# Optimization experiments

Hardware: AMD Instinct MI355X
Metric: run time of the kernel (lower is better)

Reference implementation:

```python
import jax, jax.numpy as jnp
import numpy as np

# Module constants (from init_kwargs + mp_num=8 from the mesh)
D_MODEL = 1024
N_HEAD = 16
D_HEAD = 64
D_ROT = 64
MP = 8
B, S = 2, 2048
LOCAL = N_HEAD * D_HEAD // MP          # 128 : per-mp-shard qkv dim
F_IN = N_HEAD * D_HEAD * 3 + D_MODEL * 8  # 11264 : fused qkv+ff projection width
D_OUT_IN = D_MODEL + 4 * D_MODEL       # 5120 : attn (1024) + glu (4096) into output_proj
LN_EPS = 1e-5


def _rotate_every_two(x):
    # x: [..., d] with d even -> interleaved (-x2, x1)
    x1 = x[..., ::2]
    x2 = x[..., 1::2]
    return jnp.stack((-x2, x1), axis=-1).reshape(*x.shape[:-1], -1)


def _fixed_pos_embedding(seq_len, dim):
    inv_freq = 1.0 / (10000.0 ** (np.arange(0, dim, 2) / dim))
    t = np.einsum('i,j->ij', np.arange(seq_len), inv_freq)  # [S, dim//2]
    return jnp.asarray(np.sin(t), jnp.float32), jnp.asarray(np.cos(t), jnp.float32)


def _apply_rotary(x, sin, cos):
    # x: [B, S, mp, D_ROT]; sin/cos: [S, D_ROT//2]
    sin = jnp.repeat(sin, 2, axis=-1)[-x.shape[-3]:, None, :]  # [S,1,D_ROT]
    cos = jnp.repeat(cos, 2, axis=-1)[-x.shape[-3]:, None, :]
    return x * cos + _rotate_every_two(x) * sin


def setup_inputs() -> dict:
    key = jax.random.key(0)
    ks = jax.random.split(key, 4)
    x = jax.random.normal(ks[0], (B, S, D_MODEL), jnp.float32)
    attn_bias = jnp.zeros((1, S, S), jnp.float32)
    ln_scale = jnp.ones((D_MODEL,), jnp.float32)
    ln_offset = jnp.zeros((D_MODEL,), jnp.float32)
    w_in = jax.random.normal(ks[1], (D_MODEL, F_IN), jnp.float32) / np.sqrt(D_MODEL)
    b_in = jnp.zeros((F_IN,), jnp.float32)
    w_out = jax.random.normal(ks[2], (D_OUT_IN, D_MODEL), jnp.float32) / np.sqrt(D_MODEL)
    b_out = jnp.zeros((D_MODEL,), jnp.float32)
    return {"x": x, "attn_bias": attn_bias, "ln_scale": ln_scale, "ln_offset": ln_offset,
            "w_in": w_in, "b_in": b_in, "w_out": w_out, "b_out": b_out}


def reference(x, attn_bias, ln_scale, ln_offset, w_in, b_in, w_out, b_out):
    b, s, d = x.shape
    # LayerNorm (create_scale=True, create_offset=True, eps=1e-5)
    mu = jnp.mean(x, axis=-1, keepdims=True)
    var = jnp.var(x, axis=-1, keepdims=True)
    h = (x - mu) * jax.lax.rsqrt(var + LN_EPS) * ln_scale + ln_offset
    # fused QKV + FF projection, then mp split: [B,S,mp,F_IN/mp]
    proj = (h @ w_in + b_in).reshape(b, s, MP, -1)
    q, v, k, ff = jnp.split(proj, [LOCAL, 2 * LOCAL, 3 * LOCAL], axis=-1)
    # rotary on the first D_ROT dims of each mp shard (head_split is a shape no-op)
    sin, cos = _fixed_pos_embedding(s, D_ROT)
    q = jnp.concatenate([_apply_rotary(q[..., :D_ROT], sin, cos), q[..., D_ROT:]], axis=-1)
    k = jnp.concatenate([_apply_rotary(k[..., :D_ROT], sin, cos), k[..., D_ROT:]], axis=-1)
    # attention over h=mp shard-heads of dim LOCAL; scaled by sqrt(d_head) per source
    scale = np.sqrt(D_HEAD).astype(x.dtype)
    logits = jnp.einsum('bthd,bThd->bhtT', q, k) / scale  # [B,MP,S,S]
    causal = jnp.tril(jnp.ones((s, s), x.dtype))[None]
    bias = -1e10 * (1.0 - causal) + attn_bias
    weights = jax.nn.softmax(logits + bias, axis=-1)
    attn_vec = jnp.einsum('bhtT,bThd->bthd', weights, v)  # [B,S,MP,LOCAL]
    # GLU FFN (jax.nn.gelu default = tanh approximation, as in source)
    ff_out, ff_gate = jnp.split(ff, 2, axis=-1)
    glu = ff_out * jax.nn.gelu(ff_gate)  # [B,S,MP,4*D_MODEL/MP]
    # output: concat per-shard then flatten -> output_proj
    out = jnp.concatenate([attn_vec, glu], axis=-1).reshape(b, s, -1)  # [B,S,5120]
    return out @ w_out + b_out
```

## Files before the change

kernel.cpp:

```cpp
#include <hip/hip_runtime.h>
#include <stdint.h>

#define B_   2
#define S_   2048
#define DM   1024
#define FIN  11264
#define DOUT 5120
#define NSH  8
#define DH   128
#define ROWS (B_*S_)

typedef __attribute__((ext_vector_type(8))) __bf16 bf16x8;
typedef __attribute__((ext_vector_type(4))) __bf16 bf16x4;
typedef __attribute__((ext_vector_type(4))) float  f32x4;

union U2 { unsigned int u; __bf16 h[2]; };

__device__ __forceinline__ void gload16(const void* g, void* l) {
    __builtin_amdgcn_global_load_lds((const __attribute__((address_space(1))) void*)g,
                                     (__attribute__((address_space(3))) void*)l, 16, 0, 0);
}

__global__ __launch_bounds__(256) void ln_kernel(const float* __restrict__ x,
                                                 const float* __restrict__ sc,
                                                 const float* __restrict__ of,
                                                 __bf16* __restrict__ h) {
    int row = blockIdx.x, t = threadIdx.x;
    const float4 v = *(const float4*)&x[(size_t)row*DM + t*4];
    float s  = v.x + v.y + v.z + v.w;
    float ss = v.x*v.x + v.y*v.y + v.z*v.z + v.w*v.w;
#pragma unroll
    for (int off = 32; off >= 1; off >>= 1) {
        s  += __shfl_xor(s, off);
        ss += __shfl_xor(ss, off);
    }
    __shared__ float rs_[4], rss_[4];
    int wid = t >> 6, lane = t & 63;
    if (lane == 0) { rs_[wid] = s; rss_[wid] = ss; }
    __syncthreads();
    s  = rs_[0] + rs_[1] + rs_[2] + rs_[3];
    ss = rss_[0] + rss_[1] + rss_[2] + rss_[3];
    float mu  = s * (1.f/DM);
    float var = ss * (1.f/DM) - mu*mu;
    float r   = rsqrtf(var + 1e-5f);
    float4 scv = *(const float4*)&sc[t*4];
    float4 ofv = *(const float4*)&of[t*4];
    bf16x4 o;
    o[0] = (__bf16)((v.x-mu)*r*scv.x + ofv.x);
    o[1] = (__bf16)((v.y-mu)*r*scv.y + ofv.y);
    o[2] = (__bf16)((v.z-mu)*r*scv.z + ofv.z);
    o[3] = (__bf16)((v.w-mu)*r*scv.w + ofv.w);
    *(bf16x4*)&h[(size_t)row*DM + t*4] = o;
}

__global__ __launch_bounds__(256) void transpose_kernel(const float* __restrict__ in,
                                                        __bf16* __restrict__ out,
                                                        int R, int C) {
    __shared__ __bf16 tile[64][72];
    int c0 = blockIdx.x * 64, r0 = blockIdx.y * 64;
    int t = threadIdx.x;
#pragma unroll
    for (int it = 0; it < 4; ++it) {
        int flat = it*1024 + t*4;
        int rl = flat >> 6, cl = flat & 63;
        float4 v = *(const float4*)&in[(size_t)(r0+rl)*C + c0 + cl];
        tile[rl][cl+0] = (__bf16)v.x;
        tile[rl][cl+1] = (__bf16)v.y;
        tile[rl][cl+2] = (__bf16)v.z;
        tile[rl][cl+3] = (__bf16)v.w;
    }
    __syncthreads();
#pragma unroll
    for (int it = 0; it < 4; ++it) {
        int flat = it*1024 + t*4;
        int cl = flat >> 6, rl = flat & 63;
        bf16x4 o;
#pragma unroll
        for (int j = 0; j < 4; ++j) o[j] = tile[rl+j][cl];
        *(bf16x4*)&out[(size_t)(c0+cl)*R + r0 + rl] = o;
    }
}

__global__ __launch_bounds__(256) void vtrans_kernel(const __bf16* __restrict__ in,
                                                     __bf16* __restrict__ out) {
    __shared__ __bf16 tile[64*72];
    int d0 = blockIdx.x*64, s0 = blockIdx.y*64;
    size_t base = (size_t)blockIdx.z * (size_t)S_ * DH;
    int t = threadIdx.x;
#pragma unroll
    for (int it = 0; it < 2; ++it) {
        int idx = it*2048 + t*8;
        int sl = idx >> 6, dl = idx & 63;
        bf16x8 v = *(const bf16x8*)&in[base + (size_t)(s0+sl)*DH + d0+dl];
        int ch = ((dl>>3) ^ (sl&7) ^ ((sl>>3)&7)) & 7;
        *(bf16x8*)&tile[sl*72 + ch*8] = v;
    }
    __syncthreads();
#pragma unroll
    for (int it = 0; it < 2; ++it) {
        int idx = it*2048 + t*8;
        int dl = idx >> 6, sl = idx & 63;
        bf16x8 o;
#pragma unroll
        for (int j = 0; j < 8; ++j) {
            int r = sl + j;
            int ch = ((dl>>3) ^ (r&7) ^ ((r>>3)&7)) & 7;
            o[j] = tile[r*72 + ch*8 + (dl&7)];
        }
        *(bf16x8*)&out[base + (size_t)(d0+dl)*S_ + s0 + sl] = o;
    }
}

__global__ __launch_bounds__(512, 2) void gemm256_kernel(const __bf16* __restrict__ A,
                                                         const __bf16* __restrict__ BT,
                                                         const float* __restrict__ bias,
                                                         __bf16* __restrict__ Cb,
                                                         float* __restrict__ Cf,
                                                         int M, int N, int K, int klen) {
    __shared__ __align__(16) char lds[131072];
    int t = threadIdx.x, wid = t >> 6, lane = t & 63;
    int wr = wid >> 2, wc = wid & 3;
    int fr = lane & 15, fq = lane >> 4;
    int kbeg = blockIdx.z * klen;
    int nbx = gridDim.x;
    int bid = blockIdx.y * nbx + blockIdx.x;
    int cpx = (nbx * gridDim.y) >> 3;
    int swz = (bid & 7) * cpx + (bid >> 3);
    int bx = swz % nbx, by = swz / nbx;
    int m0 = by * 256, n0 = bx * 256;

    const __bf16* pA[2];
    const __bf16* pB[2];
#pragma unroll
    for (int j = 0; j < 2; ++j) {
        int F = j*8192 + t*16;
        int row = F >> 6;
        int co  = (F & 63) ^ (((F >> 7) & 3) << 4);
        pA[j] = A  + (size_t)(m0 + row) * K + kbeg + (co >> 1);
        pB[j] = BT + (size_t)(n0 + row) * K + kbeg + (co >> 1);
    }
    int offA[8], offB[4];
#pragma unroll
    for (int i = 0; i < 8; ++i) {
        int row = wr*128 + i*16 + fr;
        offA[i] = row*64 + ((fq*16) ^ (((row >> 1) & 3) << 4));
    }
#pragma unroll
    for (int n = 0; n < 4; ++n) {
        int row = wc*64 + n*16 + fr;
        offB[n] = 16384 + row*64 + ((fq*16) ^ (((row >> 1) & 3) << 4));
    }

    f32x4 acc[8][4] = {};
    gload16(pA[0],      lds +     0 + wid*1024);
    gload16(pA[1],      lds +  8192 + wid*1024);
    gload16(pB[0],      lds + 16384 + wid*1024);
    gload16(pB[1],      lds + 24576 + wid*1024);
    gload16(pA[0] + 32, lds + 32768 +     0 + wid*1024);
    gload16(pA[1] + 32, lds + 32768 +  8192 + wid*1024);
    gload16(pB[0] + 32, lds + 32768 + 16384 + wid*1024);
    gload16(pB[1] + 32, lds + 32768 + 24576 + wid*1024);
    asm volatile("s_waitcnt vmcnt(4)" ::: "memory");
    __builtin_amdgcn_s_barrier();

    int NT = klen >> 5;
    for (int tt = 0; tt < NT; ++tt) {
        const char* sb = lds + (tt & 3) * 32768;
        bool pf = (tt + 2 < NT);
        char* sn = lds + ((tt + 2) & 3) * 32768;
        int ko = (tt + 2) << 5;
        bf16x8 a[4], b[4];
#pragma unroll
        for (int n = 0; n < 4; ++n) b[n] = *(const bf16x8*)(sb + offB[n]);
#pragma unroll
        for (int i = 0; i < 4; ++i) a[i] = *(const bf16x8*)(sb + offA[i]);
        if (pf) {
            gload16(pA[0] + ko, sn +        wid*1024);
            gload16(pA[1] + ko, sn + 8192 + wid*1024);
        }
        __builtin_amdgcn_s_barrier();
        asm volatile("s_waitcnt lgkmcnt(0)");
        __builtin_amdgcn_s_setprio(1);
#pragma unroll
        for (int i = 0; i < 4; ++i)
#pragma unroll
            for (int n = 0; n < 4; ++n)
                acc[i][n] = __builtin_amdgcn_mfma_f32_16x16x32_bf16(a[i], b[n], acc[i][n], 0, 0, 0);
        __builtin_amdgcn_s_setprio(0);
        __builtin_amdgcn_s_barrier();
#pragma unroll
        for (int i = 0; i < 4; ++i) a[i] = *(const bf16x8*)(sb + offA[4 + i]);
        if (pf) {
            gload16(pB[0] + ko, sn + 16384 + wid*1024);
            gload16(pB[1] + ko, sn + 24576 + wid*1024);
        }
        __builtin_amdgcn_s_barrier();
        asm volatile("s_waitcnt lgkmcnt(0)");
        __builtin_amdgcn_s_setprio(1);
#pragma unroll
        for (int i = 0; i < 4; ++i)
#pragma unroll
            for (int n = 0; n < 4; ++n)
                acc[4+i][n] = __builtin_amdgcn_mfma_f32_16x16x32_bf16(a[i], b[n], acc[4+i][n], 0, 0, 0);
        __builtin_amdgcn_s_setprio(0);
        if (pf)               asm volatile("s_waitcnt vmcnt(4)" ::: "memory");
        else if (tt + 1 < NT) asm volatile("s_waitcnt vmcnt(0)" ::: "memory");
        if (tt + 1 < NT) __builtin_amdgcn_s_barrier();
    }
    if (Cb) {
#pragma unroll
        for (int i = 0; i < 8; ++i)
#pragma unroll
            for (int n = 0; n < 4; ++n) {
                int col = n0 + wc*64 + n*16 + fr;
                float bv = bias[col];
#pragma unroll
                for (int r = 0; r < 4; ++r) {
                    int row = m0 + wr*128 + i*16 + fq*4 + r;
                    Cb[(size_t)row*N + col] = (__bf16)(acc[i][n][r] + bv);
                }
            }
    } else {
        float* Cz = Cf + (size_t)blockIdx.z * M * N;
#pragma unroll
        for (int i = 0; i < 8; ++i)
#pragma unroll
            for (int n = 0; n < 4; ++n) {
                int col = n0 + wc*64 + n*16 + fr;
#pragma unroll
                for (int r = 0; r < 4; ++r) {
                    int row = m0 + wr*128 + i*16 + fq*4 + r;
                    Cz[(size_t)row*N + col] = acc[i][n][r];
                }
            }
    }
}

__global__ __launch_bounds__(256) void addbias_kernel(const float* __restrict__ pk,
                                                      const float* __restrict__ bias,
                                                      float* __restrict__ out) {
    int idx = blockIdx.x * 256 + threadIdx.x;
    const size_t stride = (size_t)ROWS * DM / 4;
    float4 a0 = ((const float4*)pk)[idx];
    float4 a1 = ((const float4*)pk)[idx + stride];
    float4 a2 = ((const float4*)pk)[idx + 2*stride];
    float4 a3 = ((const float4*)pk)[idx + 3*stride];
    float4 bb = ((const float4*)bias)[idx & 255];
    float4 o;
    o.x = a0.x + a1.x + a2.x + a3.x + bb.x;
    o.y = a0.y + a1.y + a2.y + a3.y + bb.y;
    o.z = a0.z + a1.z + a2.z + a3.z + bb.z;
    o.w = a0.w + a1.w + a2.w + a3.w + bb.w;
    ((float4*)out)[idx] = o;
}

__global__ __launch_bounds__(256) void qkv_rope_kernel(const __bf16* __restrict__ proj,
                                                       __bf16* __restrict__ qh,
                                                       __bf16* __restrict__ kh,
                                                       __bf16* __restrict__ vh) {
    int idx = blockIdx.x * 256 + threadIdx.x;
    int i   = idx & 63;
    int p   = (idx >> 6) & 7;
    int row = idx >> 9;
    int s   = row & (S_ - 1);
    int b   = row >> 11;
    const __bf16* base = proj + (size_t)row*FIN + p*1408;
    int d0 = i*2;
    U2 uq, uv, uk;
    uq.u = *(const unsigned int*)&base[d0];
    uv.u = *(const unsigned int*)&base[128+d0];
    uk.u = *(const unsigned int*)&base[256+d0];
    float q0 = uq.h[0], q1 = uq.h[1];
    float v0 = uv.h[0], v1 = uv.h[1];
    float k0 = uk.h[0], k1 = uk.h[1];
    if (d0 < 64) {
        float inv = exp2f(-(float)i * 0.4152410118609203f);
        float ang = (float)s * inv;
        float cn = __cosf(ang), sn = __sinf(ang);
        float a;
        a = q0*cn - q1*sn; q1 = q1*cn + q0*sn; q0 = a;
        a = k0*cn - k1*sn; k1 = k1*cn + k0*sn; k0 = a;
    }
    size_t o = ((size_t)((b*NSH + p)*S_ + s))*DH + d0;
    U2 oq, ok, ov;
    oq.h[0] = (__bf16)(q0*0.125f); oq.h[1] = (__bf16)(q1*0.125f);
    ok.h[0] = (__bf16)k0;          ok.h[1] = (__bf16)k1;
    ov.h[0] = (__bf16)v0;          ov.h[1] = (__bf16)v1;
    *(unsigned int*)&qh[o] = oq.u;
    *(unsigned int*)&kh[o] = ok.u;
    *(unsigned int*)&vh[o] = ov.u;
}

__global__ __launch_bounds__(256) void glu_kernel(const __bf16* __restrict__ proj,
                                                  __bf16* __restrict__ ag) {
    int idx = blockIdx.x * 256 + threadIdx.x;
    int j2  = (idx & 255) * 2;
    int p   = (idx >> 8) & 7;
    int row = idx >> 11;
    const __bf16* bp = proj + (size_t)row*FIN + p*1408;
    U2 xo, xg, o;
    xo.u = *(const unsigned int*)&bp[384 + j2];
    xg.u = *(const unsigned int*)&bp[896 + j2];
#pragma unroll
    for (int j = 0; j < 2; ++j) {
        float g = xg.h[j];
        float e2 = __expf(1.5957691216057308f*(g + 0.044715f*g*g*g));
        float gl = g * (1.f - 1.f/(e2 + 1.f));
        o.h[j] = (__bf16)((float)xo.h[j] * gl);
    }
    *(unsigned int*)&ag[(size_t)row*DOUT + p*640 + 128 + j2] = o.u;
}

__device__ __forceinline__ void stage_kv(const __bf16* Kb, const __bf16* Vg,
                                         char* KsB, char* VsB,
                                         int kvbase, int t, int wid) {
#pragma unroll
    for (int j = 0; j < 4; ++j) {
        int F = (j*256 + t)*16;
        int r = F >> 8, c = F & 255;
        gload16(Kb + (size_t)(kvbase + r)*DH + ((c ^ ((r & 7) << 4)) >> 1),
                KsB + j*4096 + (wid << 10));
    }
#pragma unroll
    for (int j = 0; j < 4; ++j) {
        int F = (j*256 + t)*16;
        int r = F >> 7, c = F & 127;
        gload16(Vg + (size_t)r*S_ + kvbase + ((c ^ ((r & 7) << 4)) >> 1),
                VsB + j*4096 + (wid << 10));
    }
}

__global__ __launch_bounds__(256, 2) void attn_kernel(const __bf16* __restrict__ qh,
                                                      const __bf16* __restrict__ kh,
                                                      const __bf16* __restrict__ vt,
                                                      const float* __restrict__ ab,
                                                      __bf16* __restrict__ ag) {
    __shared__ __bf16 Ks[2*8192];
    __shared__ __bf16 Vs[2*8192];
    __shared__ __bf16 Ps[4][16*72];
    int bh = blockIdx.y;
    int b = bh >> 3, hh = bh & 7;
    int xr = blockIdx.x;
    int qb = (xr & 1) ? (31 - (xr >> 1)) : (xr >> 1);
    int q0 = qb * 64;
    int t = threadIdx.x, wid = t >> 6, lane = t & 63;
    int fr = lane & 15, fkb = (lane >> 4) * 16;
    const __bf16* Qb = qh + (size_t)bh * S_ * DH;
    const __bf16* Kb = kh + (size_t)bh * S_ * DH;
    const __bf16* Vg = vt + (size_t)bh * DH * S_;
    bf16x8 qf[4];
#pragma unroll
    for (int kk = 0; kk < 4; ++kk)
        qf[kk] = *(const bf16x8*)&Qb[(size_t)(q0 + wid*16 + fr)*DH + kk*32 + (lane>>4)*8];
    float m[4] = {-3e38f, -3e38f, -3e38f, -3e38f};
    float l[4] = {0.f, 0.f, 0.f, 0.f};
    f32x4 o[8] = {};
    int rowb = q0 + wid*16 + (lane >> 4)*4;
    int nit = qb + 1;
    stage_kv(Kb, Vg, (char*)Ks, (char*)Vs, 0, t, wid);
    for (int it = 0; it < nit; ++it) {
        int kv0 = it * 64, cur = it & 1;
        float abv[4][4];
#pragma unroll
        for (int n = 0; n < 4; ++n)
#pragma unroll
            for (int r = 0; r < 4; ++r)
                abv[n][r] = ab[(size_t)(rowb + r)*S_ + kv0 + n*16 + fr];
        if (it + 1 < nit) {
            stage_kv(Kb, Vg, (char*)Ks + (cur^1)*16384, (char*)Vs + (cur^1)*16384,
                     kv0 + 64, t, wid);
            asm volatile("s_waitcnt vmcnt(8)" ::: "memory");
        } else {
            asm volatile("s_waitcnt vmcnt(0)" ::: "memory");
        }
        __builtin_amdgcn_s_barrier();
        const char* KsC = (const char*)Ks + cur*16384;
        float pv[4][4];
        __builtin_amdgcn_s_setprio(1);
#pragma unroll
        for (int n = 0; n < 4; ++n) {
            f32x4 sacc = {};
#pragma unroll
            for (int kk = 0; kk < 4; ++kk) {
                int row = n*16 + fr;
                int c2 = (kk*64 + fkb) ^ ((fr & 7) << 4);
                bf16x8 kf = *(const bf16x8*)(KsC + row*256 + c2);
                sacc = __builtin_amdgcn_mfma_f32_16x16x32_bf16(qf[kk], kf, sacc, 0, 0, 0);
            }
#pragma unroll
            for (int r = 0; r < 4; ++r) pv[n][r] = sacc[r];
        }
        __builtin_amdgcn_s_setprio(0);
#pragma unroll
        for (int n = 0; n < 4; ++n) {
            int col = kv0 + n*16 + fr;
#pragma unroll
            for (int r = 0; r < 4; ++r)
                pv[n][r] += abv[n][r] + (col <= rowb + r ? 0.f : -1e10f);
        }
        float alpha[4];
#pragma unroll
        for (int r = 0; r < 4; ++r) {
            float mx = fmaxf(fmaxf(pv[0][r], pv[1][r]), fmaxf(pv[2][r], pv[3][r]));
#pragma unroll
            for (int off = 8; off >= 1; off >>= 1) mx = fmaxf(mx, __shfl_xor(mx, off));
            float mn = fmaxf(m[r], mx);
            alpha[r] = __expf(m[r] - mn);
            m[r] = mn;
            float sum = 0.f;
#pragma unroll
            for (int n = 0; n < 4; ++n) { pv[n][r] = __expf(pv[n][r] - mn); sum += pv[n][r]; }
#pragma unroll
            for (int off = 8; off >= 1; off >>= 1) sum += __shfl_xor(sum, off);
            l[r] = l[r]*alpha[r] + sum;
        }
#pragma unroll
        for (int nf = 0; nf < 8; ++nf)
#pragma unroll
            for (int r = 0; r < 4; ++r) o[nf][r] *= alpha[r];
#pragma unroll
        for (int n = 0; n < 4; ++n)
#pragma unroll
            for (int r = 0; r < 4; ++r)
                Ps[wid][((lane >> 4)*4 + r)*72 + n*16 + fr] = (__bf16)pv[n][r];
        asm volatile("s_waitcnt lgkmcnt(0)" ::: "memory");
        __builtin_amdgcn_sched_barrier(0);
        bf16x8 pf[2];
#pragma unroll
        for (int kk = 0; kk < 2; ++kk)
            pf[kk] = *(const bf16x8*)&Ps[wid][fr*72 + kk*32 + (lane>>4)*8];
        const char* VsC = (const char*)Vs + cur*16384;
        __builtin_amdgcn_s_setprio(1);
#pragma unroll
        for (int nf = 0; nf < 8; ++nf) {
#pragma unroll
            for (int kk = 0; kk < 2; ++kk) {
                int row = nf*16 + fr;
                int c2 = (kk*64 + fkb) ^ ((fr & 7) << 4);
                bf16x8 vf = *(const bf16x8*)(VsC + row*128 + c2);
                o[nf] = __builtin_amdgcn_mfma_f32_16x16x32_bf16(pf[kk], vf, o[nf], 0, 0, 0);
            }
        }
        __builtin_amdgcn_s_setprio(0);
        asm volatile("s_waitcnt lgkmcnt(0)" ::: "memory");
        __builtin_amdgcn_sched_barrier(0);
        __builtin_amdgcn_s_barrier();
    }
    int rq = (lane >> 4) * 4;
#pragma unroll
    for (int r = 0; r < 4; ++r) {
        float inv = 1.f / l[r];
#pragma unroll
        for (int nf = 0; nf < 8; ++nf) {
            int qr = q0 + wid*16 + rq + r;
            int d = nf*16 + fr;
            ag[((size_t)(b*S_ + qr))*DOUT + hh*640 + d] = (__bf16)(o[nf][r] * inv);
        }
    }
}

extern "C" void kernel_launch(void* const* d_in, const int* in_sizes, int n_in,
                              void* d_out, int out_size, void* d_ws, size_t ws_size,
                              hipStream_t stream) {
    const float* x     = (const float*)d_in[0];
    const float* ab    = (const float*)d_in[1];
    const float* lns   = (const float*)d_in[2];
    const float* lno   = (const float*)d_in[3];
    const float* w_in  = (const float*)d_in[4];
    const float* b_in  = (const float*)d_in[5];
    const float* w_out = (const float*)d_in[6];
    const float* b_out = (const float*)d_in[7];
    float* out = (float*)d_out;
    char* ws = (char*)d_ws;

    __bf16* w_in_t  = (__bf16*)(ws);
    __bf16* w_out_t = (__bf16*)(ws +  23068672);
    __bf16* hbuf    = (__bf16*)(ws +  33554432);
    __bf16* proj    = (__bf16*)(ws +  41943040);
    __bf16* vtb     = (__bf16*)(ws +  41943040);
    float*  pk      = (float*)(ws +  52428800);
    __bf16* qh      = (__bf16*)(ws + 134217728);
    __bf16* kh      = (__bf16*)(ws + 142606336);
    __bf16* vh      = (__bf16*)(ws + 150994944);
    __bf16* agb     = (__bf16*)(ws + 159383552);

    transpose_kernel<<<dim3(FIN/64, DM/64), 256, 0, stream>>>(w_in, w_in_t, DM, FIN);
    transpose_kernel<<<dim3(DM/64, DOUT/64), 256, 0, stream>>>(w_out, w_out_t, DOUT, DM);
    ln_kernel<<<ROWS, 256, 0, stream>>>(x, lns, lno, hbuf);
    gemm256_kernel<<<dim3(FIN/256, ROWS/256, 1), 512, 0, stream>>>(hbuf, w_in_t, b_in,
                                                                   proj, nullptr,
                                                                   ROWS, FIN, DM, DM);
    qkv_rope_kernel<<<(ROWS*8*64)/256, 256, 0, stream>>>(proj, qh, kh, vh);
    glu_kernel<<<(ROWS*8*256)/256, 256, 0, stream>>>(proj, agb);
    vtrans_kernel<<<dim3(DH/64, S_/64, B_*NSH), 256, 0, stream>>>(vh, vtb);
    attn_kernel<<<dim3(S_/64, B_*NSH), 256, 0, stream>>>(qh, kh, vtb, ab, agb);
    gemm256_kernel<<<dim3(DM/256, ROWS/256, 4), 512, 0, stream>>>(agb, w_out_t, nullptr,
                                                                  nullptr, pk,
                                                                  ROWS, DM, DOUT, DOUT/4);
    addbias_kernel<<<ROWS*DM/1024, 256, 0, stream>>>(pk, b_out, out);
}
```

Measured before the change: 319.8 us.

## Replace 256x256 pipelined GEMM with simpler 128x128 single-buffered GEMM

Result: slower. 340.4 us (+6.4%).

```diff
diff --git a/kernel.cpp b/kernel.cpp
--- a/kernel.cpp
+++ b/kernel.cpp
@@ -111,15 +111,15 @@
     }
 }
 
-__global__ __launch_bounds__(512, 2) void gemm256_kernel(const __bf16* __restrict__ A,
+__global__ __launch_bounds__(256, 4) void gemm128_kernel(const __bf16* __restrict__ A,
                                                          const __bf16* __restrict__ BT,
                                                          const float* __restrict__ bias,
                                                          __bf16* __restrict__ Cb,
                                                          float* __restrict__ Cf,
                                                          int M, int N, int K, int klen) {
-    __shared__ __align__(16) char lds[131072];
+    __shared__ __align__(16) char lds[32768];
     int t = threadIdx.x, wid = t >> 6, lane = t & 63;
-    int wr = wid >> 2, wc = wid & 3;
+    int wm = (wid >> 1) * 64, wn = (wid & 1) * 64;
     int fr = lane & 15, fq = lane >> 4;
     int kbeg = blockIdx.z * klen;
     int nbx = gridDim.x;
@@ -127,109 +127,82 @@
     int cpx = (nbx * gridDim.y) >> 3;
     int swz = (bid & 7) * cpx + (bid >> 3);
     int bx = swz % nbx, by = swz / nbx;
-    int m0 = by * 256, n0 = bx * 256;
-
-    const __bf16* pA[2];
-    const __bf16* pB[2];
-#pragma unroll
-    for (int j = 0; j < 2; ++j) {
-        int F = j*8192 + t*16;
-        int row = F >> 6;
-        int co  = (F & 63) ^ (((F >> 7) & 3) << 4);
-        pA[j] = A  + (size_t)(m0 + row) * K + kbeg + (co >> 1);
-        pB[j] = BT + (size_t)(n0 + row) * K + kbeg + (co >> 1);
-    }
-    int offA[8], offB[4];
-#pragma unroll
-    for (int i = 0; i < 8; ++i) {
-        int row = wr*128 + i*16 + fr;
-        offA[i] = row*64 + ((fq*16) ^ (((row >> 1) & 3) << 4));
-    }
-#pragma unroll
-    for (int n = 0; n < 4; ++n) {
-        int row = wc*64 + n*16 + fr;
-        offB[n] = 16384 + row*64 + ((fq*16) ^ (((row >> 1) & 3) << 4));
-    }
-
-    f32x4 acc[8][4] = {};
-    gload16(pA[0],      lds +     0 + wid*1024);
-    gload16(pA[1],      lds +  8192 + wid*1024);
-    gload16(pB[0],      lds + 16384 + wid*1024);
-    gload16(pB[1],      lds + 24576 + wid*1024);
-    gload16(pA[0] + 32, lds + 32768 +     0 + wid*1024);
-    gload16(pA[1] + 32, lds + 32768 +  8192 + wid*1024);
-    gload16(pB[0] + 32, lds + 32768 + 16384 + wid*1024);
-    gload16(pB[1] + 32, lds + 32768 + 24576 + wid*1024);
-    asm volatile("s_waitcnt vmcnt(4)" ::: "memory");
-    __builtin_amdgcn_s_barrier();
-
-    int NT = klen >> 5;
-    for (int tt = 0; tt < NT; ++tt) {
-        const char* sb = lds + (tt & 3) * 32768;
-        bool pf = (tt + 2 < NT);
-        char* sn = lds + ((tt + 2) & 3) * 32768;
-        int ko = (tt + 2) << 5;
+    int m0 = by * 128, n0 = bx * 128;
+
+    const __bf16* srcA[4];
+    const __bf16* srcB[4];
+#pragma unroll
+    for (int j = 0; j < 4; ++j) {
+        int F = (j*256 + t) * 16;
+        int row = F >> 7;
+        int c = (F & 127) ^ ((row & 7) << 4);
+        srcA[j] = A  + (size_t)(m0 + row) * K + kbeg + (c >> 1);
+        srcB[j] = BT + (size_t)(n0 + row) * K + kbeg + (c >> 1);
+    }
+    int rowA[4], rowB[4];
+#pragma unroll
+    for (int i = 0; i < 4; ++i) {
+        rowA[i] = (wm + i*16 + fr) * 128;
+        rowB[i] = 16384 + (wn + i*16 + fr) * 128;
+    }
+    int swzb = (fr & 7) << 4;
+    int cb0 = (fq*16) ^ swzb;
+    int cb1 = (64 + fq*16) ^ swzb;
+
+    f32x4 acc[4][4] = {};
+    for (int k0 = 0; k0 < klen; k0 += 64) {
+#pragma unroll
+        for (int j = 0; j < 4; ++j)
+            gload16(srcA[j] + k0, lds + j*4096 + wid*1024);
+#pragma unroll
+        for (int j = 0; j < 4; ++j)
+            gload16(srcB[j] + k0, lds + 16384 + j*4096 + wid*1024);
+        __syncthreads();
         bf16x8 a[4], b[4];
 #pragma unroll
-        for (int n = 0; n < 4; ++n) b[n] = *(const bf16x8*)(sb + offB[n]);
-#pragma unroll
-        for (int i = 0; i < 4; ++i) a[i] = *(const bf16x8*)(sb + offA[i]);
-        if (pf) {
-            gload16(pA[0] + ko, sn +        wid*1024);
-            gload16(pA[1] + ko, sn + 8192 + wid*1024);
-        }
-        __builtin_amdgcn_s_barrier();
-        asm volatile("s_waitcnt lgkmcnt(0)");
-        __builtin_amdgcn_s_setprio(1);
+        for (int i = 0; i < 4; ++i) a[i] = *(const bf16x8*)(lds + rowA[i] + cb0);
+#pragma unroll
+        for (int n = 0; n < 4; ++n) b[n] = *(const bf16x8*)(lds + rowB[n] + cb0);
 #pragma unroll
         for (int i = 0; i < 4; ++i)
 #pragma unroll
             for (int n = 0; n < 4; ++n)
                 acc[i][n] = __builtin_amdgcn_mfma_f32_16x16x32_bf16(a[i], b[n], acc[i][n], 0, 0, 0);
-        __builtin_amdgcn_s_setprio(0);
-        __builtin_amdgcn_s_barrier();
-#pragma unroll
-        for (int i = 0; i < 4; ++i) a[i] = *(const bf16x8*)(sb + offA[4 + i]);
-        if (pf) {
-            gload16(pB[0] + ko, sn + 16384 + wid*1024);
-            gload16(pB[1] + ko, sn + 24576 + wid*1024);
-        }
-        __builtin_amdgcn_s_barrier();
-        asm volatile("s_waitcnt lgkmcnt(0)");
-        __builtin_amdgcn_s_setprio(1);
+#pragma unroll
+        for (int i = 0; i < 4; ++i) a[i] = *(const bf16x8*)(lds + rowA[i] + cb1);
+#pragma unroll
+        for (int n = 0; n < 4; ++n) b[n] = *(const bf16x8*)(lds + rowB[n] + cb1);
 #pragma unroll
         for (int i = 0; i < 4; ++i)
 #pragma unroll
             for (int n = 0; n < 4; ++n)
-                acc[4+i][n] = __builtin_amdgcn_mfma_f32_16x16x32_bf16(a[i], b[n], acc[4+i][n], 0, 0, 0);
-        __builtin_amdgcn_s_setprio(0);
-        if (pf)               asm volatile("s_waitcnt vmcnt(4)" ::: "memory");
-        else if (tt + 1 < NT) asm volatile("s_waitcnt vmcnt(0)" ::: "memory");
-        if (tt + 1 < NT) __builtin_amdgcn_s_barrier();
-    }
+                acc[i][n] = __builtin_amdgcn_mfma_f32_16x16x32_bf16(a[i], b[n], acc[i][n], 0, 0, 0);
+        __syncthreads();
+    }
+    int rq = fq * 4;
     if (Cb) {
 #pragma unroll
-        for (int i = 0; i < 8; ++i)
+        for (int i = 0; i < 4; ++i)
 #pragma unroll
             for (int n = 0; n < 4; ++n) {
-                int col = n0 + wc*64 + n*16 + fr;
+                int col = n0 + wn + n*16 + fr;
                 float bv = bias[col];
 #pragma unroll
                 for (int r = 0; r < 4; ++r) {
-                    int row = m0 + wr*128 + i*16 + fq*4 + r;
+                    int row = m0 + wm + i*16 + rq + r;
                     Cb[(size_t)row*N + col] = (__bf16)(acc[i][n][r] + bv);
                 }
             }
     } else {
         float* Cz = Cf + (size_t)blockIdx.z * M * N;
 #pragma unroll
-        for (int i = 0; i < 8; ++i)
+        for (int i = 0; i < 4; ++i)
 #pragma unroll
             for (int n = 0; n < 4; ++n) {
-                int col = n0 + wc*64 + n*16 + fr;
+                int col = n0 + wn + n*16 + fr;
 #pragma unroll
                 for (int r = 0; r < 4; ++r) {
-                    int row = m0 + wr*128 + i*16 + fq*4 + r;
+                    int row = m0 + wm + i*16 + rq + r;
                     Cz[(size_t)row*N + col] = acc[i][n][r];
                 }
             }
@@ -487,14 +460,14 @@
     transpose_kernel<<<dim3(FIN/64, DM/64), 256, 0, stream>>>(w_in, w_in_t, DM, FIN);
     transpose_kernel<<<dim3(DM/64, DOUT/64), 256, 0, stream>>>(w_out, w_out_t, DOUT, DM);
     ln_kernel<<<ROWS, 256, 0, stream>>>(x, lns, lno, hbuf);
-    gemm256_kernel<<<dim3(FIN/256, ROWS/256, 1), 512, 0, stream>>>(hbuf, w_in_t, b_in,
+    gemm128_kernel<<<dim3(FIN/128, ROWS/128, 1), 256, 0, stream>>>(hbuf, w_in_t, b_in,
                                                                    proj, nullptr,
                                                                    ROWS, FIN, DM, DM);
     qkv_rope_kernel<<<(ROWS*8*64)/256, 256, 0, stream>>>(proj, qh, kh, vh);
     glu_kernel<<<(ROWS*8*256)/256, 256, 0, stream>>>(proj, agb);
     vtrans_kernel<<<dim3(DH/64, S_/64, B_*NSH), 256, 0, stream>>>(vh, vtb);
     attn_kernel<<<dim3(S_/64, B_*NSH), 256, 0, stream>>>(qh, kh, vtb, ab, agb);
-    gemm256_kernel<<<dim3(DM/256, ROWS/256, 4), 512, 0, stream>>>(agb, w_out_t, nullptr,
+    gemm128_kernel<<<dim3(DM/128, ROWS/128, 4), 256, 0, stream>>>(agb, w_out_t, nullptr,
                                                                   nullptr, pk,
                                                                   ROWS, DM, DOUT, DOUT/4);
     addbias_kernel<<<ROWS*DM/1024, 256, 0, stream>>>(pk, b_out, out);
```
